# Kernel tuning notes

Hardware: AMD Instinct MI355X
Metric: run time of the kernel (lower is better)

The kernel has to match this reference:

```python
import jax, jax.numpy as jnp
import numpy as np

N_NODES = 100000
N_EDGES = 3200000
IN_CH, HID, OUT_CH = 512, 16, 64


def gcn_conv(x, src, dst, W, b, n_nodes):
    """GCNConv: x @ W, then sym-normalized aggregation with self-loops."""
    xw = x @ W  # [N, F_out]
    loop = jnp.arange(n_nodes, dtype=src.dtype)
    s = jnp.concatenate([src, loop])  # sources (messages gathered here)
    d = jnp.concatenate([dst, loop])  # targets (messages scattered here)
    deg = jax.ops.segment_sum(jnp.ones_like(d, dtype=xw.dtype), d, num_segments=n_nodes)
    dinv = jnp.where(deg > 0, jax.lax.rsqrt(deg), 0.0)
    norm = dinv[s] * dinv[d]  # [E+N]
    msgs = xw[s] * norm[:, None]  # gather + scale
    out = jax.ops.segment_sum(msgs, d, num_segments=n_nodes)
    return out + b


def setup_inputs() -> dict:
    key = jax.random.key(0)
    k1, k2, k3, k4, k5 = jax.random.split(key, 5)
    x = jax.random.normal(k1, (N_NODES, IN_CH), dtype=jnp.float32)
    edge_index = jax.random.randint(k2, (2, N_EDGES), 0, N_NODES, dtype=jnp.int32)
    # Glorot-style init for GCNConv linear weights, zero bias (PyG default)
    W1 = jax.random.normal(k3, (IN_CH, HID), dtype=jnp.float32) * (1.0 / np.sqrt(IN_CH))
    b1 = jnp.zeros((HID,), dtype=jnp.float32)
    W2 = jax.random.normal(k4, (HID, OUT_CH), dtype=jnp.float32) * (1.0 / np.sqrt(HID))
    b2 = jnp.zeros((OUT_CH,), dtype=jnp.float32)
    return {"x": x, "edge_index": edge_index, "W1": W1, "b1": b1, "W2": W2, "b2": b2}


def reference(x, edge_index, W1, b1, W2, b2):
    # eval mode: dropout(p=0.5) is identity
    src, dst = edge_index[0], edge_index[1]
    h = gcn_conv(x, src, dst, W1, b1, N_NODES)
    h = jax.nn.relu(h)
    out = gcn_conv(h, src, dst, W2, b2, N_NODES)
    return out
```

## Files before the change

kernel.cpp:

```cpp
#include <hip/hip_runtime.h>

#define N_NODES 100000
#define N_EDGES 3200000
#define IN_CH 512
#define HID 16
#define OUT_CH 64

#define NB1 98
#define CAP1 34816
#define LEAF 64
#define CAP2 2560
#define NLEAF 1563
#define NLEAF_SLOTS (NB1 * 16)
#define BIN1_CHUNK 4096
#define BIN1_BLOCKS ((N_EDGES + BIN1_CHUNK - 1) / BIN1_CHUNK)
#define BIN2_SPLIT 9
#define BIN2_CHUNK 3872

typedef float f4 __attribute__((ext_vector_type(4)));
typedef unsigned int v2u __attribute__((ext_vector_type(2)));

__device__ __forceinline__ unsigned rne(float f) {
    unsigned u = __float_as_uint(f);
    return (u + 0x7fffu + ((u >> 16) & 1u)) >> 16;
}
__device__ __forceinline__ v2u pk4(f4 f) {
    v2u r;
    r.x = rne(f.x) | (rne(f.y) << 16);
    r.y = rne(f.z) | (rne(f.w) << 16);
    return r;
}
__device__ __forceinline__ f4 up4(v2u v) {
    f4 r;
    r.x = __uint_as_float(v.x << 16);
    r.y = __uint_as_float(v.x & 0xffff0000u);
    r.z = __uint_as_float(v.y << 16);
    r.w = __uint_as_float(v.y & 0xffff0000u);
    return r;
}


__global__ void k_init_bcur(int* bcur1, int* bcur2, int* off) {
    int i = blockIdx.x * blockDim.x + threadIdx.x;
    if (i < NB1) bcur1[i] = i * CAP1;
    if (i < NLEAF_SLOTS) bcur2[i] = i * CAP2;
    if (i == 0) off[N_NODES] = N_EDGES;
}


__global__ __launch_bounds__(256) void k_bin1(const int* __restrict__ src,
                                              const int* __restrict__ dst,
                                              int* __restrict__ pairs1,
                                              int* __restrict__ bcur1) {
    __shared__ int cnt[NB1];
    __shared__ int base[NB1];
    const int tid = threadIdx.x;
    const int lo = blockIdx.x * BIN1_CHUNK;
    const int hi = min(lo + BIN1_CHUNK, N_EDGES);
    if (tid < NB1) cnt[tid] = 0;
    __syncthreads();
    for (int i = lo + tid; i < hi; i += 256) {
        int d = __builtin_nontemporal_load(dst + i);
        atomicAdd(&cnt[d >> 10], 1);
    }
    __syncthreads();
    if (tid < NB1 && cnt[tid] > 0) base[tid] = atomicAdd(&bcur1[tid], cnt[tid]);
    __syncthreads();
    if (tid < NB1) cnt[tid] = 0;
    __syncthreads();
    for (int i = lo + tid; i < hi; i += 256) {
        int d = __builtin_nontemporal_load(dst + i);
        int s = __builtin_nontemporal_load(src + i);
        int b = d >> 10;
        int r = atomicAdd(&cnt[b], 1);
        pairs1[base[b] + r] = (s << 10) | (d & 1023);
    }
}


__global__ __launch_bounds__(256) void k_bin2(const int* __restrict__ pairs1,
                                              const int* __restrict__ bcur1,
                                              int* __restrict__ pairs2,
                                              int* __restrict__ bcur2) {
    __shared__ int cnt[16];
    __shared__ int base[16];
    const int b = blockIdx.x / BIN2_SPLIT;
    const int s = blockIdx.x % BIN2_SPLIT;
    const int tid = threadIdx.x;
    const int len = bcur1[b] - b * CAP1;
    const int lo = b * CAP1 + min(s * BIN2_CHUNK, len);
    const int hi = b * CAP1 + min((s + 1) * BIN2_CHUNK, len);
    if (tid < 16) cnt[tid] = 0;
    __syncthreads();
    for (int i = lo + tid; i < hi; i += 256)
        atomicAdd(&cnt[(pairs1[i] & 1023) >> 6], 1);
    __syncthreads();
    if (tid < 16 && cnt[tid] > 0) base[tid] = atomicAdd(&bcur2[b * 16 + tid], cnt[tid]);
    __syncthreads();
    if (tid < 16) cnt[tid] = 0;
    __syncthreads();
    for (int i = lo + tid; i < hi; i += 256) {
        int e = pairs1[i];
        int l = (e & 1023) >> 6;
        int r = atomicAdd(&cnt[l], 1);
        pairs2[base[l] + r] = e;
    }
}


__global__ __launch_bounds__(256) void k_leafscan(const int* __restrict__ bcur2,
                                                  int* __restrict__ leafoff) {
    __shared__ int sm[256];
    __shared__ int carry;
    const int tid = threadIdx.x;
    if (tid == 0) carry = 0;
    __syncthreads();
    for (int r = 0; r < (NLEAF_SLOTS + 255) / 256; ++r) {
        int idx = r * 256 + tid;
        int v = (idx < NLEAF_SLOTS) ? (bcur2[idx] - idx * CAP2) : 0;
        sm[tid] = v;
        __syncthreads();
        for (int st = 1; st < 256; st <<= 1) {
            int t = (tid >= st) ? sm[tid - st] : 0;
            __syncthreads();
            sm[tid] += t;
            __syncthreads();
        }
        if (idx < NLEAF_SLOTS) leafoff[idx] = carry + sm[tid] - v;
        int tot = sm[255];
        __syncthreads();
        if (tid == 0) carry += tot;
        __syncthreads();
    }
}


__global__ __launch_bounds__(256) void k_scatter2(const int* __restrict__ pairs2,
                                                  const int* __restrict__ bcur2,
                                                  const int* __restrict__ leafoff,
                                                  int* __restrict__ off,
                                                  float* __restrict__ dinv,
                                                  int* __restrict__ csr) {
    __shared__ int cnt[LEAF];
    __shared__ int lcur[LEAF];
    __shared__ int buf[CAP2];
    const int leaf = blockIdx.x;
    const int tid = threadIdx.x;
    const int base2 = leaf * CAP2;
    const int len = min(bcur2[leaf] - base2, CAP2);
    const int obase = leafoff[leaf];
    if (tid < LEAF) cnt[tid] = 0;
    __syncthreads();
    for (int i = tid; i < len; i += 256)
        atomicAdd(&cnt[pairs2[base2 + i] & 63], 1);
    __syncthreads();
    if (tid < LEAF) {
        int v = cnt[tid];
        int s = v;
        for (int d = 1; d < LEAF; d <<= 1) {
            int t = __shfl_up(s, d, 64);
            if (tid >= d) s += t;
        }
        int excl = s - v;
        lcur[tid] = excl;
        int node = leaf * LEAF + tid;
        if (node < N_NODES) {
            off[node] = obase + excl;
            dinv[node] = rsqrtf((float)(1 + v));
        }
    }
    __syncthreads();
    for (int i = tid; i < len; i += 256) {
        int e = pairs2[base2 + i];
        int p = atomicAdd(&lcur[e & 63], 1);
        buf[p] = e >> 10;
    }
    __syncthreads();
    for (int i = tid; i < len; i += 256)
        csr[obase + i] = buf[i];
}


#define G1_BS 256
#define G1_NODES 128
#define G1_KT 64
#define G1_STRIDE (G1_KT + 4)

__global__ __launch_bounds__(G1_BS) void k_gemm1(const float* __restrict__ x,
                                                 const float* __restrict__ W1,
                                                 const float* __restrict__ dinv,
                                                 unsigned short* __restrict__ y1) {
    __shared__ float xt[G1_NODES * G1_STRIDE];
    __shared__ float wt[G1_KT * HID];
    const int tid = threadIdx.x;
    const int nl = tid >> 2;
    const int cg = tid & 3;
    const int node_base = blockIdx.x * G1_NODES;

    f4 acc0 = {0.f, 0.f, 0.f, 0.f};
    f4 acc1 = {0.f, 0.f, 0.f, 0.f};

    for (int kt = 0; kt < IN_CH; kt += G1_KT) {
        __syncthreads();
        for (int j = 0; j < 8; ++j) {
            int f = j * G1_BS + tid;
            int r = f >> 4;
            int c4 = f & 15;
            int gr = node_base + r;
            f4 v = {0.f, 0.f, 0.f, 0.f};
            if (gr < N_NODES)
                v = *(const f4*)(x + (size_t)gr * IN_CH + kt + c4 * 4);
            *(f4*)(xt + r * G1_STRIDE + c4 * 4) = v;
        }
        {
            int r = tid >> 2;
            int c4 = tid & 3;
            *(f4*)(wt + r * HID + c4 * 4) =
                *(const f4*)(W1 + (size_t)(kt + r) * HID + c4 * 4);
        }
        __syncthreads();

        for (int kk = 0; kk < G1_KT; kk += 4) {
            f4 x0 = *(const f4*)(xt + nl * G1_STRIDE + kk);
            f4 x1 = *(const f4*)(xt + (nl + 64) * G1_STRIDE + kk);
            f4 w0 = *(const f4*)(wt + (kk + 0) * HID + cg * 4);
            f4 w1 = *(const f4*)(wt + (kk + 1) * HID + cg * 4);
            f4 w2 = *(const f4*)(wt + (kk + 2) * HID + cg * 4);
            f4 w3 = *(const f4*)(wt + (kk + 3) * HID + cg * 4);
            acc0 += x0.x * w0; acc0 += x0.y * w1;
            acc0 += x0.z * w2; acc0 += x0.w * w3;
            acc1 += x1.x * w0; acc1 += x1.y * w1;
            acc1 += x1.z * w2; acc1 += x1.w * w3;
        }
    }

    int n0 = node_base + nl;
    int n1 = n0 + 64;
    if (n0 < N_NODES) {
        float dv = dinv[n0];
        __builtin_nontemporal_store(pk4(acc0 * dv),
            (v2u*)(y1 + (size_t)n0 * HID + cg * 4));
    }
    if (n1 < N_NODES) {
        float dv = dinv[n1];
        __builtin_nontemporal_store(pk4(acc1 * dv),
            (v2u*)(y1 + (size_t)n1 * HID + cg * 4));
    }
}


__global__ __launch_bounds__(256) void k_layer1(const unsigned short* __restrict__ y1,
                                                const int* __restrict__ off,
                                                const int* __restrict__ csr,
                                                const float* __restrict__ b1,
                                                unsigned short* __restrict__ y2) {
    int t = blockIdx.x * blockDim.x + threadIdx.x;
    int n = t >> 2;
    int cg = t & 3;
    if (n >= N_NODES) return;
    int base = off[n];
    int cnt = off[n + 1] - base;
    f4 a0 = {0,0,0,0}, a1 = {0,0,0,0}, a2 = {0,0,0,0}, a3 = {0,0,0,0};
    f4 a4 = {0,0,0,0}, a5 = {0,0,0,0}, a6 = {0,0,0,0}, a7 = {0,0,0,0};
    int p = 0;
    for (; p + 8 <= cnt; p += 8) {
        int s0 = csr[base + p + 0];
        int s1 = csr[base + p + 1];
        int s2 = csr[base + p + 2];
        int s3 = csr[base + p + 3];
        int s4 = csr[base + p + 4];
        int s5 = csr[base + p + 5];
        int s6 = csr[base + p + 6];
        int s7 = csr[base + p + 7];
        a0 += up4(*(const v2u*)(y1 + (size_t)s0 * HID + cg * 4));
        a1 += up4(*(const v2u*)(y1 + (size_t)s1 * HID + cg * 4));
        a2 += up4(*(const v2u*)(y1 + (size_t)s2 * HID + cg * 4));
        a3 += up4(*(const v2u*)(y1 + (size_t)s3 * HID + cg * 4));
        a4 += up4(*(const v2u*)(y1 + (size_t)s4 * HID + cg * 4));
        a5 += up4(*(const v2u*)(y1 + (size_t)s5 * HID + cg * 4));
        a6 += up4(*(const v2u*)(y1 + (size_t)s6 * HID + cg * 4));
        a7 += up4(*(const v2u*)(y1 + (size_t)s7 * HID + cg * 4));
    }
    for (; p < cnt; ++p)
        a0 += up4(*(const v2u*)(y1 + (size_t)csr[base + p] * HID + cg * 4));
    f4 acc = ((a0 + a1) + (a2 + a3)) + ((a4 + a5) + (a6 + a7));
    float dv = rsqrtf((float)(cnt + 1));
    f4 self = up4(*(const v2u*)(y1 + (size_t)n * HID + cg * 4));
    f4 b = ((const f4*)b1)[cg];
    f4 h;
    h.x = fmaxf(dv * (acc.x + self.x) + b.x, 0.f) * dv;
    h.y = fmaxf(dv * (acc.y + self.y) + b.y, 0.f) * dv;
    h.z = fmaxf(dv * (acc.z + self.z) + b.z, 0.f) * dv;
    h.w = fmaxf(dv * (acc.w + self.w) + b.w, 0.f) * dv;
    __builtin_nontemporal_store(pk4(h), (v2u*)(y2 + (size_t)n * HID + cg * 4));
}


__global__ __launch_bounds__(256) void k_layer2(const unsigned short* __restrict__ y2,
                                                const int* __restrict__ off,
                                                const int* __restrict__ csr,
                                                const float* __restrict__ W2,
                                                const float* __restrict__ b2,
                                                float* __restrict__ out) {
    __shared__ float w2[HID * OUT_CH];
    __shared__ float bs[OUT_CH];
    int tid = threadIdx.x;
    for (int j = tid; j < HID * OUT_CH; j += 256) w2[j] = W2[j];
    if (tid < OUT_CH) bs[tid] = b2[tid];
    __syncthreads();

    int t = blockIdx.x * blockDim.x + tid;
    int n = t >> 2;
    int cg = t & 3;
    if (n >= N_NODES) return;
    int base = off[n];
    int cnt = off[n + 1] - base;
    f4 a0 = {0,0,0,0}, a1 = {0,0,0,0}, a2 = {0,0,0,0}, a3 = {0,0,0,0};
    f4 a4 = {0,0,0,0}, a5 = {0,0,0,0}, a6 = {0,0,0,0}, a7 = {0,0,0,0};
    int p = 0;
    for (; p + 8 <= cnt; p += 8) {
        int s0 = csr[base + p + 0];
        int s1 = csr[base + p + 1];
        int s2 = csr[base + p + 2];
        int s3 = csr[base + p + 3];
        int s4 = csr[base + p + 4];
        int s5 = csr[base + p + 5];
        int s6 = csr[base + p + 6];
        int s7 = csr[base + p + 7];
        a0 += up4(*(const v2u*)(y2 + (size_t)s0 * HID + cg * 4));
        a1 += up4(*(const v2u*)(y2 + (size_t)s1 * HID + cg * 4));
        a2 += up4(*(const v2u*)(y2 + (size_t)s2 * HID + cg * 4));
        a3 += up4(*(const v2u*)(y2 + (size_t)s3 * HID + cg * 4));
        a4 += up4(*(const v2u*)(y2 + (size_t)s4 * HID + cg * 4));
        a5 += up4(*(const v2u*)(y2 + (size_t)s5 * HID + cg * 4));
        a6 += up4(*(const v2u*)(y2 + (size_t)s6 * HID + cg * 4));
        a7 += up4(*(const v2u*)(y2 + (size_t)s7 * HID + cg * 4));
    }
    for (; p < cnt; ++p)
        a0 += up4(*(const v2u*)(y2 + (size_t)csr[base + p] * HID + cg * 4));
    f4 acc = ((a0 + a1) + (a2 + a3)) + ((a4 + a5) + (a6 + a7));
    float dv = rsqrtf((float)(cnt + 1));
    f4 self = up4(*(const v2u*)(y2 + (size_t)n * HID + cg * 4));
    f4 z4 = {dv * (acc.x + self.x), dv * (acc.y + self.y),
             dv * (acc.z + self.z), dv * (acc.w + self.w)};

    int lane = tid & 63;
    int lbase = lane & ~3;
    float z[16];
#pragma unroll
    for (int j = 0; j < 4; ++j) {
        z[j * 4 + 0] = __shfl(z4.x, lbase + j, 64);
        z[j * 4 + 1] = __shfl(z4.y, lbase + j, 64);
        z[j * 4 + 2] = __shfl(z4.z, lbase + j, 64);
        z[j * 4 + 3] = __shfl(z4.w, lbase + j, 64);
    }

    f4 o0 = ((const f4*)bs)[cg * 4 + 0];
    f4 o1 = ((const f4*)bs)[cg * 4 + 1];
    f4 o2 = ((const f4*)bs)[cg * 4 + 2];
    f4 o3 = ((const f4*)bs)[cg * 4 + 3];
#pragma unroll
    for (int cc = 0; cc < HID; ++cc) {
        const float* wr = w2 + cc * OUT_CH + cg * 16;
        float zz = z[cc];
        o0 += zz * *(const f4*)(wr + 0);
        o1 += zz * *(const f4*)(wr + 4);
        o2 += zz * *(const f4*)(wr + 8);
        o3 += zz * *(const f4*)(wr + 12);
    }
    float* orow = out + (size_t)n * OUT_CH + cg * 16;
    __builtin_nontemporal_store(o0, (f4*)(orow + 0));
    __builtin_nontemporal_store(o1, (f4*)(orow + 4));
    __builtin_nontemporal_store(o2, (f4*)(orow + 8));
    __builtin_nontemporal_store(o3, (f4*)(orow + 12));
}


extern "C" void kernel_launch(void* const* d_in, const int* in_sizes, int n_in,
                              void* d_out, int out_size, void* d_ws, size_t ws_size,
                              hipStream_t stream) {
    const float* x  = (const float*)d_in[0];
    const int*   ei = (const int*)d_in[1];
    const float* W1 = (const float*)d_in[2];
    const float* b1 = (const float*)d_in[3];
    const float* W2 = (const float*)d_in[4];
    const float* b2 = (const float*)d_in[5];
    float* out = (float*)d_out;

    const int* src = ei;
    const int* dst = ei + N_EDGES;

    char* w = (char*)d_ws;
    const size_t SN = 409600;
    float* dinv     = (float*)(w);
    int*   off      = (int*)(w + SN);
    int*   bcur1    = (int*)(w + 2 * SN);
    int*   bcur2    = (int*)(w + 2 * SN + 8192);
    int*   leafoff  = (int*)(w + 2 * SN + 16384);
    char*  regB     = w + 3 * SN;
    int*   pairs1   = (int*)regB;
    int*   csr      = (int*)regB;
    char*  regC     = regB + (size_t)NB1 * CAP1 * 4;
    int*   pairs2   = (int*)regC;
    unsigned short* y1 = (unsigned short*)regC;
    unsigned short* y2 = (unsigned short*)(regC + 3200000);

    k_init_bcur<<<(NLEAF_SLOTS + 255) / 256, 256, 0, stream>>>(bcur1, bcur2, off);
    k_bin1<<<BIN1_BLOCKS, 256, 0, stream>>>(src, dst, pairs1, bcur1);
    k_bin2<<<NB1 * BIN2_SPLIT, 256, 0, stream>>>(pairs1, bcur1, pairs2, bcur2);
    k_leafscan<<<1, 256, 0, stream>>>(bcur2, leafoff);
    k_scatter2<<<NLEAF, 256, 0, stream>>>(pairs2, bcur2, leafoff, off, dinv, csr);
    k_gemm1<<<(N_NODES + G1_NODES - 1) / G1_NODES, G1_BS, 0, stream>>>(x, W1, dinv, y1);
    k_layer1<<<(N_NODES * 4 + 255) / 256, 256, 0, stream>>>(y1, off, csr, b1, y2);
    k_layer2<<<(N_NODES * 4 + 255) / 256, 256, 0, stream>>>(y2, off, csr, W2, b2, out);
}
```

Baseline: 205.8 us.

## Fuse CSR-build preprocessing kernels into one cooperative grid-synced kernel

Merges the init, two binning passes, leaf scan and leaf scatter kernels into a single cooperative launch of 1024 persistent blocks. The stages are separated by grid.sync() instead of kernel boundaries, and shared memory is reused between stages. The aim is to remove the launch gaps and tail drain between the five small kernels. In exchange it pays for four grid-wide barriers, runs grid-stride loops over a fixed grid, and needs every block to be co-resident. Local variables named cg are renamed so they do not clash with the cooperative_groups namespace alias.

```diff
diff --git a/kernel.cpp b/kernel.cpp
--- a/kernel.cpp
+++ b/kernel.cpp
@@ -1,4 +1,7 @@
 #include <hip/hip_runtime.h>
+#include <hip/hip_cooperative_groups.h>
+
+namespace cg = cooperative_groups;
 
 #define N_NODES 100000
 #define N_EDGES 3200000
@@ -16,6 +19,7 @@
 #define BIN1_BLOCKS ((N_EDGES + BIN1_CHUNK - 1) / BIN1_CHUNK)
 #define BIN2_SPLIT 9
 #define BIN2_CHUNK 3872
+#define CHAIN_GRID 1024
 
 typedef float f4 __attribute__((ext_vector_type(4)));
 typedef unsigned int v2u __attribute__((ext_vector_type(2)));
@@ -40,144 +44,141 @@
 }
 
 
-__global__ void k_init_bcur(int* bcur1, int* bcur2, int* off) {
-    int i = blockIdx.x * blockDim.x + threadIdx.x;
-    if (i < NB1) bcur1[i] = i * CAP1;
-    if (i < NLEAF_SLOTS) bcur2[i] = i * CAP2;
-    if (i == 0) off[N_NODES] = N_EDGES;
-}
-
-
-__global__ __launch_bounds__(256) void k_bin1(const int* __restrict__ src,
-                                              const int* __restrict__ dst,
-                                              int* __restrict__ pairs1,
-                                              int* __restrict__ bcur1) {
-    __shared__ int cnt[NB1];
-    __shared__ int base[NB1];
+__global__ __launch_bounds__(256) void k_chain(const int* __restrict__ src,
+                                               const int* __restrict__ dst,
+                                               int* __restrict__ pairs1,
+                                               int* __restrict__ bcur1,
+                                               int* __restrict__ pairs2,
+                                               int* __restrict__ bcur2,
+                                               int* __restrict__ leafoff,
+                                               int* __restrict__ off,
+                                               float* __restrict__ dinv,
+                                               int* __restrict__ csr) {
+    cg::grid_group grid = cg::this_grid();
+    __shared__ int sm[2688];
     const int tid = threadIdx.x;
-    const int lo = blockIdx.x * BIN1_CHUNK;
-    const int hi = min(lo + BIN1_CHUNK, N_EDGES);
-    if (tid < NB1) cnt[tid] = 0;
-    __syncthreads();
-    for (int i = lo + tid; i < hi; i += 256) {
-        int d = __builtin_nontemporal_load(dst + i);
-        atomicAdd(&cnt[d >> 10], 1);
-    }
-    __syncthreads();
-    if (tid < NB1 && cnt[tid] > 0) base[tid] = atomicAdd(&bcur1[tid], cnt[tid]);
-    __syncthreads();
-    if (tid < NB1) cnt[tid] = 0;
-    __syncthreads();
-    for (int i = lo + tid; i < hi; i += 256) {
-        int d = __builtin_nontemporal_load(dst + i);
-        int s = __builtin_nontemporal_load(src + i);
-        int b = d >> 10;
-        int r = atomicAdd(&cnt[b], 1);
-        pairs1[base[b] + r] = (s << 10) | (d & 1023);
-    }
-}
-
-
-__global__ __launch_bounds__(256) void k_bin2(const int* __restrict__ pairs1,
-                                              const int* __restrict__ bcur1,
-                                              int* __restrict__ pairs2,
-                                              int* __restrict__ bcur2) {
-    __shared__ int cnt[16];
-    __shared__ int base[16];
-    const int b = blockIdx.x / BIN2_SPLIT;
-    const int s = blockIdx.x % BIN2_SPLIT;
-    const int tid = threadIdx.x;
-    const int len = bcur1[b] - b * CAP1;
-    const int lo = b * CAP1 + min(s * BIN2_CHUNK, len);
-    const int hi = b * CAP1 + min((s + 1) * BIN2_CHUNK, len);
-    if (tid < 16) cnt[tid] = 0;
-    __syncthreads();
-    for (int i = lo + tid; i < hi; i += 256)
-        atomicAdd(&cnt[(pairs1[i] & 1023) >> 6], 1);
-    __syncthreads();
-    if (tid < 16 && cnt[tid] > 0) base[tid] = atomicAdd(&bcur2[b * 16 + tid], cnt[tid]);
-    __syncthreads();
-    if (tid < 16) cnt[tid] = 0;
-    __syncthreads();
-    for (int i = lo + tid; i < hi; i += 256) {
-        int e = pairs1[i];
-        int l = (e & 1023) >> 6;
-        int r = atomicAdd(&cnt[l], 1);
-        pairs2[base[l] + r] = e;
-    }
-}
-
-
-__global__ __launch_bounds__(256) void k_leafscan(const int* __restrict__ bcur2,
-                                                  int* __restrict__ leafoff) {
-    __shared__ int sm[256];
-    __shared__ int carry;
-    const int tid = threadIdx.x;
-    if (tid == 0) carry = 0;
-    __syncthreads();
-    for (int r = 0; r < (NLEAF_SLOTS + 255) / 256; ++r) {
-        int idx = r * 256 + tid;
-        int v = (idx < NLEAF_SLOTS) ? (bcur2[idx] - idx * CAP2) : 0;
-        sm[tid] = v;
-        __syncthreads();
-        for (int st = 1; st < 256; st <<= 1) {
-            int t = (tid >= st) ? sm[tid - st] : 0;
+
+    for (int i = blockIdx.x * 256 + tid; i < NLEAF_SLOTS; i += CHAIN_GRID * 256) {
+        if (i < NB1) bcur1[i] = i * CAP1;
+        bcur2[i] = i * CAP2;
+    }
+    if (blockIdx.x == 0 && tid == 0) off[N_NODES] = N_EDGES;
+    grid.sync();
+
+    for (int blk = blockIdx.x; blk < BIN1_BLOCKS; blk += CHAIN_GRID) {
+        int* cnt = sm;
+        int* base = sm + NB1;
+        const int lo = blk * BIN1_CHUNK;
+        const int hi = min(lo + BIN1_CHUNK, N_EDGES);
+        __syncthreads();
+        if (tid < NB1) cnt[tid] = 0;
+        __syncthreads();
+        for (int i = lo + tid; i < hi; i += 256) {
+            int d = __builtin_nontemporal_load(dst + i);
+            atomicAdd(&cnt[d >> 10], 1);
+        }
+        __syncthreads();
+        if (tid < NB1 && cnt[tid] > 0) base[tid] = atomicAdd(&bcur1[tid], cnt[tid]);
+        __syncthreads();
+        if (tid < NB1) cnt[tid] = 0;
+        __syncthreads();
+        for (int i = lo + tid; i < hi; i += 256) {
+            int d = __builtin_nontemporal_load(dst + i);
+            int s = __builtin_nontemporal_load(src + i);
+            int b = d >> 10;
+            int r = atomicAdd(&cnt[b], 1);
+            pairs1[base[b] + r] = (s << 10) | (d & 1023);
+        }
+    }
+    grid.sync();
+
+    for (int vb = blockIdx.x; vb < NB1 * BIN2_SPLIT; vb += CHAIN_GRID) {
+        int* cnt = sm;
+        int* base = sm + 16;
+        const int b = vb / BIN2_SPLIT;
+        const int s = vb % BIN2_SPLIT;
+        const int len = bcur1[b] - b * CAP1;
+        const int lo = b * CAP1 + min(s * BIN2_CHUNK, len);
+        const int hi = b * CAP1 + min((s + 1) * BIN2_CHUNK, len);
+        __syncthreads();
+        if (tid < 16) cnt[tid] = 0;
+        __syncthreads();
+        for (int i = lo + tid; i < hi; i += 256)
+            atomicAdd(&cnt[(pairs1[i] & 1023) >> 6], 1);
+        __syncthreads();
+        if (tid < 16 && cnt[tid] > 0) base[tid] = atomicAdd(&bcur2[b * 16 + tid], cnt[tid]);
+        __syncthreads();
+        if (tid < 16) cnt[tid] = 0;
+        __syncthreads();
+        for (int i = lo + tid; i < hi; i += 256) {
+            int e = pairs1[i];
+            int l = (e & 1023) >> 6;
+            int r = atomicAdd(&cnt[l], 1);
+            pairs2[base[l] + r] = e;
+        }
+    }
+    grid.sync();
+
+    if (blockIdx.x == 0) {
+        int* smv = sm;
+        for (int r = 0; r < (NLEAF_SLOTS + 255) / 256; ++r) {
+            int idx = r * 256 + tid;
+            int v = (idx < NLEAF_SLOTS) ? (bcur2[idx] - idx * CAP2) : 0;
+            smv[tid] = v;
             __syncthreads();
-            sm[tid] += t;
+            for (int st = 1; st < 256; st <<= 1) {
+                int t = (tid >= st) ? smv[tid - st] : 0;
+                __syncthreads();
+                smv[tid] += t;
+                __syncthreads();
+            }
+            if (idx < NLEAF_SLOTS) leafoff[idx] = sm[2687] * (r > 0) + smv[tid] - v;
+            int tot = smv[255] + (r > 0 ? sm[2687] : 0);
             __syncthreads();
-        }
-        if (idx < NLEAF_SLOTS) leafoff[idx] = carry + sm[tid] - v;
-        int tot = sm[255];
-        __syncthreads();
-        if (tid == 0) carry += tot;
-        __syncthreads();
-    }
-}
-
-
-__global__ __launch_bounds__(256) void k_scatter2(const int* __restrict__ pairs2,
-                                                  const int* __restrict__ bcur2,
-                                                  const int* __restrict__ leafoff,
-                                                  int* __restrict__ off,
-                                                  float* __restrict__ dinv,
-                                                  int* __restrict__ csr) {
-    __shared__ int cnt[LEAF];
-    __shared__ int lcur[LEAF];
-    __shared__ int buf[CAP2];
-    const int leaf = blockIdx.x;
-    const int tid = threadIdx.x;
-    const int base2 = leaf * CAP2;
-    const int len = min(bcur2[leaf] - base2, CAP2);
-    const int obase = leafoff[leaf];
-    if (tid < LEAF) cnt[tid] = 0;
-    __syncthreads();
-    for (int i = tid; i < len; i += 256)
-        atomicAdd(&cnt[pairs2[base2 + i] & 63], 1);
-    __syncthreads();
-    if (tid < LEAF) {
-        int v = cnt[tid];
-        int s = v;
-        for (int d = 1; d < LEAF; d <<= 1) {
-            int t = __shfl_up(s, d, 64);
-            if (tid >= d) s += t;
-        }
-        int excl = s - v;
-        lcur[tid] = excl;
-        int node = leaf * LEAF + tid;
-        if (node < N_NODES) {
-            off[node] = obase + excl;
-            dinv[node] = rsqrtf((float)(1 + v));
-        }
-    }
-    __syncthreads();
-    for (int i = tid; i < len; i += 256) {
-        int e = pairs2[base2 + i];
-        int p = atomicAdd(&lcur[e & 63], 1);
-        buf[p] = e >> 10;
-    }
-    __syncthreads();
-    for (int i = tid; i < len; i += 256)
-        csr[obase + i] = buf[i];
+            if (tid == 0) sm[2687] = tot;
+            __syncthreads();
+        }
+    }
+    grid.sync();
+
+    for (int leaf = blockIdx.x; leaf < NLEAF; leaf += CHAIN_GRID) {
+        int* cnt = sm;
+        int* lcur = sm + LEAF;
+        int* buf = sm + 2 * LEAF;
+        const int base2 = leaf * CAP2;
+        const int len = min(bcur2[leaf] - base2, CAP2);
+        const int obase = leafoff[leaf];
+        __syncthreads();
+        if (tid < LEAF) cnt[tid] = 0;
+        __syncthreads();
+        for (int i = tid; i < len; i += 256)
+            atomicAdd(&cnt[pairs2[base2 + i] & 63], 1);
+        __syncthreads();
+        if (tid < LEAF) {
+            int v = cnt[tid];
+            int s = v;
+            for (int d = 1; d < LEAF; d <<= 1) {
+                int t = __shfl_up(s, d, 64);
+                if (tid >= d) s += t;
+            }
+            int excl = s - v;
+            lcur[tid] = excl;
+            int node = leaf * LEAF + tid;
+            if (node < N_NODES) {
+                off[node] = obase + excl;
+                dinv[node] = rsqrtf((float)(1 + v));
+            }
+        }
+        __syncthreads();
+        for (int i = tid; i < len; i += 256) {
+            int e = pairs2[base2 + i];
+            int p = atomicAdd(&lcur[e & 63], 1);
+            buf[p] = e >> 10;
+        }
+        __syncthreads();
+        for (int i = tid; i < len; i += 256)
+            csr[obase + i] = buf[i];
+    }
 }
 
 
@@ -194,7 +195,7 @@
     __shared__ float wt[G1_KT * HID];
     const int tid = threadIdx.x;
     const int nl = tid >> 2;
-    const int cg = tid & 3;
+    const int cg2 = tid & 3;
     const int node_base = blockIdx.x * G1_NODES;
 
     f4 acc0 = {0.f, 0.f, 0.f, 0.f};
@@ -223,10 +224,10 @@
         for (int kk = 0; kk < G1_KT; kk += 4) {
             f4 x0 = *(const f4*)(xt + nl * G1_STRIDE + kk);
             f4 x1 = *(const f4*)(xt + (nl + 64) * G1_STRIDE + kk);
-            f4 w0 = *(const f4*)(wt + (kk + 0) * HID + cg * 4);
-            f4 w1 = *(const f4*)(wt + (kk + 1) * HID + cg * 4);
-            f4 w2 = *(const f4*)(wt + (kk + 2) * HID + cg * 4);
-            f4 w3 = *(const f4*)(wt + (kk + 3) * HID + cg * 4);
+            f4 w0 = *(const f4*)(wt + (kk + 0) * HID + cg2 * 4);
+            f4 w1 = *(const f4*)(wt + (kk + 1) * HID + cg2 * 4);
+            f4 w2 = *(const f4*)(wt + (kk + 2) * HID + cg2 * 4);
+            f4 w3 = *(const f4*)(wt + (kk + 3) * HID + cg2 * 4);
             acc0 += x0.x * w0; acc0 += x0.y * w1;
             acc0 += x0.z * w2; acc0 += x0.w * w3;
             acc1 += x1.x * w0; acc1 += x1.y * w1;
@@ -239,12 +240,12 @@
     if (n0 < N_NODES) {
         float dv = dinv[n0];
         __builtin_nontemporal_store(pk4(acc0 * dv),
-            (v2u*)(y1 + (size_t)n0 * HID + cg * 4));
+            (v2u*)(y1 + (size_t)n0 * HID + cg2 * 4));
     }
     if (n1 < N_NODES) {
         float dv = dinv[n1];
         __builtin_nontemporal_store(pk4(acc1 * dv),
-            (v2u*)(y1 + (size_t)n1 * HID + cg * 4));
+            (v2u*)(y1 + (size_t)n1 * HID + cg2 * 4));
     }
 }
 
@@ -256,7 +257,7 @@
                                                 unsigned short* __restrict__ y2) {
     int t = blockIdx.x * blockDim.x + threadIdx.x;
     int n = t >> 2;
-    int cg = t & 3;
+    int cg2 = t & 3;
     if (n >= N_NODES) return;
     int base = off[n];
     int cnt = off[n + 1] - base;
@@ -272,27 +273,27 @@
         int s5 = csr[base + p + 5];
         int s6 = csr[base + p + 6];
         int s7 = csr[base + p + 7];
-        a0 += up4(*(const v2u*)(y1 + (size_t)s0 * HID + cg * 4));
-        a1 += up4(*(const v2u*)(y1 + (size_t)s1 * HID + cg * 4));
-        a2 += up4(*(const v2u*)(y1 + (size_t)s2 * HID + cg * 4));
-        a3 += up4(*(const v2u*)(y1 + (size_t)s3 * HID + cg * 4));
-        a4 += up4(*(const v2u*)(y1 + (size_t)s4 * HID + cg * 4));
-        a5 += up4(*(const v2u*)(y1 + (size_t)s5 * HID + cg * 4));
-        a6 += up4(*(const v2u*)(y1 + (size_t)s6 * HID + cg * 4));
-        a7 += up4(*(const v2u*)(y1 + (size_t)s7 * HID + cg * 4));
+        a0 += up4(*(const v2u*)(y1 + (size_t)s0 * HID + cg2 * 4));
+        a1 += up4(*(const v2u*)(y1 + (size_t)s1 * HID + cg2 * 4));
+        a2 += up4(*(const v2u*)(y1 + (size_t)s2 * HID + cg2 * 4));
+        a3 += up4(*(const v2u*)(y1 + (size_t)s3 * HID + cg2 * 4));
+        a4 += up4(*(const v2u*)(y1 + (size_t)s4 * HID + cg2 * 4));
+        a5 += up4(*(const v2u*)(y1 + (size_t)s5 * HID + cg2 * 4));
+        a6 += up4(*(const v2u*)(y1 + (size_t)s6 * HID + cg2 * 4));
+        a7 += up4(*(const v2u*)(y1 + (size_t)s7 * HID + cg2 * 4));
     }
     for (; p < cnt; ++p)
-        a0 += up4(*(const v2u*)(y1 + (size_t)csr[base + p] * HID + cg * 4));
+        a0 += up4(*(const v2u*)(y1 + (size_t)csr[base + p] * HID + cg2 * 4));
     f4 acc = ((a0 + a1) + (a2 + a3)) + ((a4 + a5) + (a6 + a7));
     float dv = rsqrtf((float)(cnt + 1));
-    f4 self = up4(*(const v2u*)(y1 + (size_t)n * HID + cg * 4));
-    f4 b = ((const f4*)b1)[cg];
+    f4 self = up4(*(const v2u*)(y1 + (size_t)n * HID + cg2 * 4));
+    f4 b = ((const f4*)b1)[cg2];
     f4 h;
     h.x = fmaxf(dv * (acc.x + self.x) + b.x, 0.f) * dv;
     h.y = fmaxf(dv * (acc.y + self.y) + b.y, 0.f) * dv;
     h.z = fmaxf(dv * (acc.z + self.z) + b.z, 0.f) * dv;
     h.w = fmaxf(dv * (acc.w + self.w) + b.w, 0.f) * dv;
-    __builtin_nontemporal_store(pk4(h), (v2u*)(y2 + (size_t)n * HID + cg * 4));
+    __builtin_nontemporal_store(pk4(h), (v2u*)(y2 + (size_t)n * HID + cg2 * 4));
 }
 
 
@@ -311,7 +312,7 @@
 
     int t = blockIdx.x * blockDim.x + tid;
     int n = t >> 2;
-    int cg = t & 3;
+    int cg2 = t & 3;
     if (n >= N_NODES) return;
     int base = off[n];
     int cnt = off[n + 1] - base;
@@ -327,20 +328,20 @@
         int s5 = csr[base + p + 5];
         int s6 = csr[base + p + 6];
         int s7 = csr[base + p + 7];
-        a0 += up4(*(const v2u*)(y2 + (size_t)s0 * HID + cg * 4));
-        a1 += up4(*(const v2u*)(y2 + (size_t)s1 * HID + cg * 4));
-        a2 += up4(*(const v2u*)(y2 + (size_t)s2 * HID + cg * 4));
-        a3 += up4(*(const v2u*)(y2 + (size_t)s3 * HID + cg * 4));
-        a4 += up4(*(const v2u*)(y2 + (size_t)s4 * HID + cg * 4));
-        a5 += up4(*(const v2u*)(y2 + (size_t)s5 * HID + cg * 4));
-        a6 += up4(*(const v2u*)(y2 + (size_t)s6 * HID + cg * 4));
-        a7 += up4(*(const v2u*)(y2 + (size_t)s7 * HID + cg * 4));
+        a0 += up4(*(const v2u*)(y2 + (size_t)s0 * HID + cg2 * 4));
+        a1 += up4(*(const v2u*)(y2 + (size_t)s1 * HID + cg2 * 4));
+        a2 += up4(*(const v2u*)(y2 + (size_t)s2 * HID + cg2 * 4));
+        a3 += up4(*(const v2u*)(y2 + (size_t)s3 * HID + cg2 * 4));
+        a4 += up4(*(const v2u*)(y2 + (size_t)s4 * HID + cg2 * 4));
+        a5 += up4(*(const v2u*)(y2 + (size_t)s5 * HID + cg2 * 4));
+        a6 += up4(*(const v2u*)(y2 + (size_t)s6 * HID + cg2 * 4));
+        a7 += up4(*(const v2u*)(y2 + (size_t)s7 * HID + cg2 * 4));
     }
     for (; p < cnt; ++p)
-        a0 += up4(*(const v2u*)(y2 + (size_t)csr[base + p] * HID + cg * 4));
+        a0 += up4(*(const v2u*)(y2 + (size_t)csr[base + p] * HID + cg2 * 4));
     f4 acc = ((a0 + a1) + (a2 + a3)) + ((a4 + a5) + (a6 + a7));
     float dv = rsqrtf((float)(cnt + 1));
-    f4 self = up4(*(const v2u*)(y2 + (size_t)n * HID + cg * 4));
+    f4 self = up4(*(const v2u*)(y2 + (size_t)n * HID + cg2 * 4));
     f4 z4 = {dv * (acc.x + self.x), dv * (acc.y + self.y),
              dv * (acc.z + self.z), dv * (acc.w + self.w)};
 
@@ -355,20 +356,20 @@
         z[j * 4 + 3] = __shfl(z4.w, lbase + j, 64);
     }
 
-    f4 o0 = ((const f4*)bs)[cg * 4 + 0];
-    f4 o1 = ((const f4*)bs)[cg * 4 + 1];
-    f4 o2 = ((const f4*)bs)[cg * 4 + 2];
-    f4 o3 = ((const f4*)bs)[cg * 4 + 3];
+    f4 o0 = ((const f4*)bs)[cg2 * 4 + 0];
+    f4 o1 = ((const f4*)bs)[cg2 * 4 + 1];
+    f4 o2 = ((const f4*)bs)[cg2 * 4 + 2];
+    f4 o3 = ((const f4*)bs)[cg2 * 4 + 3];
 #pragma unroll
     for (int cc = 0; cc < HID; ++cc) {
-        const float* wr = w2 + cc * OUT_CH + cg * 16;
+        const float* wr = w2 + cc * OUT_CH + cg2 * 16;
         float zz = z[cc];
         o0 += zz * *(const f4*)(wr + 0);
         o1 += zz * *(const f4*)(wr + 4);
         o2 += zz * *(const f4*)(wr + 8);
         o3 += zz * *(const f4*)(wr + 12);
     }
-    float* orow = out + (size_t)n * OUT_CH + cg * 16;
+    float* orow = out + (size_t)n * OUT_CH + cg2 * 16;
     __builtin_nontemporal_store(o0, (f4*)(orow + 0));
     __builtin_nontemporal_store(o1, (f4*)(orow + 4));
     __builtin_nontemporal_store(o2, (f4*)(orow + 8));
@@ -405,11 +406,11 @@
     unsigned short* y1 = (unsigned short*)regC;
     unsigned short* y2 = (unsigned short*)(regC + 3200000);
 
-    k_init_bcur<<<(NLEAF_SLOTS + 255) / 256, 256, 0, stream>>>(bcur1, bcur2, off);
-    k_bin1<<<BIN1_BLOCKS, 256, 0, stream>>>(src, dst, pairs1, bcur1);
-    k_bin2<<<NB1 * BIN2_SPLIT, 256, 0, stream>>>(pairs1, bcur1, pairs2, bcur2);
-    k_leafscan<<<1, 256, 0, stream>>>(bcur2, leafoff);
-    k_scatter2<<<NLEAF, 256, 0, stream>>>(pairs2, bcur2, leafoff, off, dinv, csr);
+    void* chain_args[] = {(void*)&src, (void*)&dst, (void*)&pairs1, (void*)&bcur1,
+                          (void*)&pairs2, (void*)&bcur2, (void*)&leafoff,
+                          (void*)&off, (void*)&dinv, (void*)&csr};
+    hipLaunchCooperativeKernel((void*)k_chain, dim3(CHAIN_GRID), dim3(256),
+                               chain_args, 0, stream);
     k_gemm1<<<(N_NODES + G1_NODES - 1) / G1_NODES, G1_BS, 0, stream>>>(x, W1, dinv, y1);
     k_layer1<<<(N_NODES * 4 + 255) / 256, 256, 0, stream>>>(y1, off, csr, b1, y2);
     k_layer2<<<(N_NODES * 4 + 255) / 256, 256, 0, stream>>>(y2, off, csr, W2, b2, out);
```

Result: slower. 610.2 us (+196.5%).
